# Performance work log

Hardware: AMD Instinct MI355X
Metric: run time of the kernel (lower is better)

Reference implementation:

```python
import jax, jax.numpy as jnp
import numpy as np

B, S, SE, D, H, F1, I, E, ND = 8, 512, 512, 1024, 16, 4096, 1024, 8, 4

def _ln(x, g, b, eps=1e-5):
    mu = x.mean(-1, keepdims=True)
    var = ((x - mu) ** 2).mean(-1, keepdims=True)
    return (x - mu) * jax.lax.rsqrt(var + eps) * g + b

def _mha(q_in, kv_in, qw, qb, kw, kb, vw, vb, ow, ob):
    b, sq, d = q_in.shape
    sk = kv_in.shape[1]
    dh = d // H
    scale = dh ** -0.5
    q = ((q_in @ qw.T + qb) * scale).reshape(b, sq, H, dh)
    k = (kv_in @ kw.T + kb).reshape(b, sk, H, dh)
    v = (kv_in @ vw.T + vb).reshape(b, sk, H, dh)
    attn = jax.nn.softmax(jnp.einsum('bqhd,bkhd->bhqk', q, k), axis=-1)
    o = jnp.einsum('bhqk,bkhd->bqhd', attn, v).reshape(b, sq, d)
    return o @ ow.T + ob

def setup_inputs():
    key = jax.random.key(0)
    ks = jax.random.split(key, 40)
    p = lambda i, sh: jax.random.normal(ks[i], sh, jnp.float32) * 0.02
    return {
        'hidden_states': jax.random.normal(ks[0], (B, S, D), jnp.float32),
        'encoder_hidden_states': jax.random.normal(ks[1], (B, SE, D), jnp.float32),
        'idxes': jax.random.randint(ks[2], (B,), 0, ND),
        'sa_qw': p(3, (D, D)), 'sa_qb': p(4, (D,)), 'sa_kw': p(5, (D, D)), 'sa_kb': p(6, (D,)),
        'sa_vw': p(7, (D, D)), 'sa_vb': p(8, (D,)), 'sa_ow': p(9, (D, D)), 'sa_ob': p(10, (D,)),
        'ca_qw': p(11, (D, D)), 'ca_qb': p(12, (D,)), 'ca_kw': p(13, (D, D)), 'ca_kb': p(14, (D,)),
        'ca_vw': p(15, (D, D)), 'ca_vb': p(16, (D,)), 'ca_ow': p(17, (D, D)), 'ca_ob': p(18, (D,)),
        'sa_ln_g': jnp.ones((D,), jnp.float32), 'sa_ln_b': jnp.zeros((D,), jnp.float32),
        'ca_ln_g': jnp.ones((D,), jnp.float32), 'ca_ln_b': jnp.zeros((D,), jnp.float32),
        'fin_ln_g': jnp.ones((D,), jnp.float32), 'fin_ln_b': jnp.zeros((D,), jnp.float32),
        'fc1_w': p(19, (F1, D)), 'fc1_b': p(20, (F1,)),
        'fc2_w': p(21, (D, F1)), 'fc2_b': p(22, (D,)),
        'exp1_w': p(23, (E, I, D)), 'exp1_b': p(24, (E, I)),
        'exp2_w': p(25, (E, D, I)),
        'gate_w': p(26, (ND, E, D)), 'gate_b': p(27, (ND, E)),
    }

def reference(hidden_states, encoder_hidden_states, idxes, sa_qw, sa_qb, sa_kw, sa_kb, sa_vw, sa_vb, sa_ow, sa_ob, ca_qw, ca_qb, ca_kw, ca_kb, ca_vw, ca_vb, ca_ow, ca_ob, sa_ln_g, sa_ln_b, ca_ln_g, ca_ln_b, fin_ln_g, fin_ln_b, fc1_w, fc1_b, fc2_w, fc2_b, exp1_w, exp1_b, exp2_w, gate_w, gate_b):
    # self-attention block
    res = hidden_states
    h = _mha(hidden_states, hidden_states, sa_qw, sa_qb, sa_kw, sa_kb, sa_vw, sa_vb, sa_ow, sa_ob)
    h = _ln(res + h, sa_ln_g, sa_ln_b)
    # cross-attention block
    res = h
    h = _mha(h, encoder_hidden_states, ca_qw, ca_qb, ca_kw, ca_kb, ca_vw, ca_vb, ca_ow, ca_ob)
    h = _ln(res + h, ca_ln_g, ca_ln_b)
    # dataset-gated MoE FFN (dropout=0 eval, margin_loss=False, keep_resident=True)
    bsz, seq, d = h.shape
    x = h.reshape(-1, d)                              # [T, D]
    tok_ds = jnp.repeat(idxes, seq)                   # [T] dataset id per token
    logits = jnp.einsum('ted,td->te', gate_w[tok_ds], x) + gate_b[tok_ds]
    probs = jax.nn.softmax(logits, axis=-1)
    gate = jnp.argmax(probs, axis=-1)                 # top-1 expert per token
    gate_value = jnp.max(probs, axis=-1)
    oh = jax.nn.one_hot(gate, E, dtype=x.dtype)       # [T, E] dispatch mask
    # effective expert fc1 = concat(fc1, expert_fc1): shared half + per-token expert half
    h1 = jax.nn.gelu(x @ fc1_w.T + fc1_b, approximate=False)                                  # [T, F1]
    h2 = jax.nn.gelu(jnp.einsum('td,te,eid->ti', x, oh, exp1_w) + exp1_b[gate], approximate=False)  # [T, I]
    # effective expert fc2 = concat(fc2, expert_fc2, dim=1), shared fc2 bias
    out = h1 @ fc2_w.T + jnp.einsum('ti,te,edi->td', h2, oh, exp2_w) + fc2_b                  # [T, D]
    out = out * gate_value[:, None]                   # keep_resident: scale before residual
    out = _ln(x + out, fin_ln_g, fin_ln_b)
    return out.reshape(bsz, seq, d)
```

## Files before the change

kernel.cpp:

```cpp
#include <hip/hip_runtime.h>
#include <math.h>

constexpr int cS = 512, cD = 1024, cH = 16, cDH = 64;
constexpr int cF1 = 4096, cI = 1024, cE = 8;
constexpr int cT = 4096;
constexpr long long TD = (long long)cT * cD;
constexpr long long WW = 1048576;

typedef __attribute__((ext_vector_type(8))) short bfrag;
typedef _Float16 f16x8 __attribute__((ext_vector_type(8)));
typedef __attribute__((ext_vector_type(4))) float f32x4;

__device__ __forceinline__ float gelu_exact(float x) {
  return 0.5f * x * (1.0f + erff(x * 0.70710678118654752440f));
}
__device__ __forceinline__ unsigned short f2b_rne(float x) {
  union { float f; unsigned u; } v; v.f = x;
  unsigned r = v.u + 0x7fffu + ((v.u >> 16) & 1u);
  return (unsigned short)(r >> 16);
}
__device__ __forceinline__ void split2(float v, unsigned short& h, unsigned short& m) {
  _Float16 hh = (_Float16)v;
  float r = v - (float)hh;
  _Float16 mm = (_Float16)r;
  union { _Float16 f; unsigned short u; } a, b;
  a.f = hh; b.f = mm;
  h = a.u; m = b.u;
}
__device__ __forceinline__ void async16(const void* g, void* l) {
  __builtin_amdgcn_global_load_lds(
      (const __attribute__((address_space(1))) unsigned int*)g,
      (__attribute__((address_space(3))) unsigned int*)l, 16, 0, 0);
}

template<int BM, int BN, int OUT_MODE, int AFP32>
__global__ __launch_bounds__(256) void mgemm2(
    const void* __restrict__ Ap, long long aPS, long long sA, int lda,
    const unsigned short* __restrict__ Bp, long long bPS, long long sB, int ldb,
    const float* __restrict__ bias,
    void* __restrict__ Cp, long long sC, int ldc,
    int K, float alpha, int zbase)
{
  constexpr int WM = BM / 2, WN = BN / 2, AI = WM / 16, BJ = WN / 16;
  constexpr int CA = AFP32 ? 0 : 2 * (BM / 16);
  constexpr int CB = 2 * (BN / 16);
  constexpr int CTOT = CA + CB;
  static_assert(CTOT % 4 == 0, "chunk count");
  constexpr int NCH = CTOT / 4;
  constexpr int FPT = (BM * 32) / 256;
  constexpr int TPR = 256 / BM;

  __shared__ unsigned short lA[2][BM * 32];
  __shared__ unsigned short lB[2][BN * 32];

  const int tid = threadIdx.x;
  const int w = tid >> 6, lane = tid & 63;
  const int z = blockIdx.z;
  const int m0 = blockIdx.x * BM, n0 = blockIdx.y * BN;
  const int wm = (w >> 1) * WM, wn = (w & 1) * WN;
  const int lr = lane >> 2, lc8 = (lane & 3) * 8;

  const unsigned short* gsrc[NCH];
  unsigned short* ldst[NCH];
#pragma unroll
  for (int ci = 0; ci < NCH; ++ci) {
    const int c = w + ci * 4;
    if (c < CA) {
      const int p = c / (BM / 16), cc = c % (BM / 16);
      const int row = cc * 16 + lr;
      gsrc[ci] = (const unsigned short*)Ap + p * aPS + (long long)z * sA
               + (long long)(m0 + row) * lda + lc8;
      ldst[ci] = &lA[p][cc * 16 * 32];
    } else {
      const int cb = c - CA;
      const int p = cb / (BN / 16), cc = cb % (BN / 16);
      const int row = cc * 16 + lr;
      gsrc[ci] = Bp + p * bPS + (long long)z * sB + (long long)(n0 + row) * ldb + lc8;
      ldst[ci] = &lB[p][cc * 16 * 32];
    }
  }
  const float* af32 = nullptr;
  int arow = 0, acol = 0;
  if constexpr (AFP32) {
    arow = tid / TPR; acol = (tid % TPR) * FPT;
    af32 = (const float*)Ap + (long long)z * sA + (long long)(m0 + arow) * lda + acol;
  }

  f32x4 acc[AI][BJ];
#pragma unroll
  for (int i = 0; i < AI; ++i)
#pragma unroll
    for (int j = 0; j < BJ; ++j) acc[i][j] = (f32x4){0.f, 0.f, 0.f, 0.f};

  for (int k0 = 0; k0 < K; k0 += 32) {
#pragma unroll
    for (int ci = 0; ci < NCH; ++ci) async16(gsrc[ci] + k0, ldst[ci]);
    if constexpr (AFP32) {
      float vv[FPT];
#pragma unroll
      for (int q4 = 0; q4 < FPT / 4; ++q4)
        *(float4*)&vv[q4 * 4] = *(const float4*)(af32 + k0 + q4 * 4);
      unsigned pk[2][FPT / 2];
#pragma unroll
      for (int q = 0; q < FPT / 2; ++q) {
        unsigned short h0, m0s, h1, m1s;
        split2(vv[2 * q], h0, m0s);
        split2(vv[2 * q + 1], h1, m1s);
        pk[0][q] = (unsigned)h0 | ((unsigned)h1 << 16);
        pk[1][q] = (unsigned)m0s | ((unsigned)m1s << 16);
      }
#pragma unroll
      for (int p = 0; p < 2; ++p) {
        unsigned* d = (unsigned*)&lA[p][arow * 32 + acol];
#pragma unroll
        for (int u = 0; u < FPT / 8; ++u)
          *(uint4*)(d + u * 4) = *(const uint4*)&pk[p][u * 4];
      }
    }
    asm volatile("s_waitcnt vmcnt(0)" ::: "memory");
    __syncthreads();

    f16x8 bf0[BJ], bf1[BJ], af[AI];
#pragma unroll
    for (int j = 0; j < BJ; ++j) {
      bf0[j] = *(const f16x8*)&lB[0][(wn + j * 16 + (lane & 15)) * 32 + (lane >> 4) * 8];
      bf1[j] = *(const f16x8*)&lB[1][(wn + j * 16 + (lane & 15)) * 32 + (lane >> 4) * 8];
    }
#pragma unroll
    for (int i = 0; i < AI; ++i)
      af[i] = *(const f16x8*)&lA[0][(wm + i * 16 + (lane & 15)) * 32 + (lane >> 4) * 8];
#pragma unroll
    for (int i = 0; i < AI; ++i)
#pragma unroll
      for (int j = 0; j < BJ; ++j)
        acc[i][j] = __builtin_amdgcn_mfma_f32_16x16x32_f16(af[i], bf0[j], acc[i][j], 0, 0, 0);
#pragma unroll
    for (int i = 0; i < AI; ++i)
#pragma unroll
      for (int j = 0; j < BJ; ++j)
        acc[i][j] = __builtin_amdgcn_mfma_f32_16x16x32_f16(af[i], bf1[j], acc[i][j], 0, 0, 0);
#pragma unroll
    for (int i = 0; i < AI; ++i)
      af[i] = *(const f16x8*)&lA[1][(wm + i * 16 + (lane & 15)) * 32 + (lane >> 4) * 8];
#pragma unroll
    for (int i = 0; i < AI; ++i)
#pragma unroll
      for (int j = 0; j < BJ; ++j)
        acc[i][j] = __builtin_amdgcn_mfma_f32_16x16x32_f16(af[i], bf0[j], acc[i][j], 0, 0, 0);
    __syncthreads();
  }

  const int zz = zbase + z;
#pragma unroll
  for (int i = 0; i < AI; ++i) {
#pragma unroll
    for (int r = 0; r < 4; ++r) {
      const int gm = m0 + wm + i * 16 + (lane >> 4) * 4 + r;
#pragma unroll
      for (int j = 0; j < BJ; ++j) {
        const int gn = n0 + wn + j * 16 + (lane & 15);
        float v = acc[i][j][r];
        if constexpr (OUT_MODE == 4) {
          v += bias[zz * cD + gn];
          unsigned short* C = (unsigned short*)Cp + (long long)zz * 2 * TD;
          const int b = gm >> 9, s = gm & 511, h = gn >> 6, dd = gn & 63;
          const long long idx = (((long long)(b * cH + h) * cS + s) << 6) + dd;
          unsigned short h_, m_;
          split2(v, h_, m_);
          C[idx] = h_; C[TD + idx] = m_;
        } else {
          if (bias) v += bias[gn];
          v *= alpha;
          long long idx;
          if constexpr (OUT_MODE == 0) {
            idx = (long long)z * sC + (long long)gm * ldc + gn;
          } else {
            const int b = zz >> 4, h = zz & 15;
            idx = ((long long)(b * cS + gm) << 10) + h * 64 + gn;
          }
          ((float*)Cp)[idx] = v;
        }
      }
    }
  }
}

__global__ __launch_bounds__(256) void transposeV(
    const unsigned short* __restrict__ src, unsigned short* __restrict__ dst)
{
  __shared__ unsigned short t[128 * 64];
  const int st = blockIdx.x;
  const int bh = blockIdx.y;
  const long long pl = (long long)blockIdx.z * TD;
  const unsigned short* Sp = src + pl + ((long long)bh * cS + st * 128) * cDH;
  const int tid = threadIdx.x;
  const int r0 = tid >> 3, c0 = (tid & 7) * 8;
#pragma unroll
  for (int i = 0; i < 4; ++i) {
    const int r = r0 + i * 32;
    uint4 v = *(const uint4*)(Sp + (long long)r * cDH + c0);
    *(uint4*)&t[r * 64 + (c0 ^ ((r & 7) << 3))] = v;
  }
  __syncthreads();
  const int dd = tid >> 2;
  unsigned short* Dp = dst + pl + (long long)(bh * cDH + dd) * cS + st * 128;
#pragma unroll
  for (int i = 0; i < 4; ++i) {
    const int s0 = ((tid & 3) + i * 4) * 8;
    alignas(16) unsigned short v[8];
#pragma unroll
    for (int j = 0; j < 8; ++j)
      v[j] = t[(s0 + j) * 64 + (dd ^ (j << 3))];
    *(uint4*)(Dp + s0) = *(const uint4*)v;
  }
}

template<int GATHER>
__global__ __launch_bounds__(256) void mgemm1(
    const unsigned short* __restrict__ A, int lda,
    const unsigned short* __restrict__ Bw, long long sB, int ldb,
    const float* __restrict__ bias, int sBias,
    void* __restrict__ Cp, int ldc,
    int K, int act, int obf, int accum,
    const int* __restrict__ token_list, const int* __restrict__ offsets)
{
  int m0, n0, beg = 0, cnt = 0x7fffffff;
  long long boff = 0;
  if constexpr (GATHER) {
    const int e = blockIdx.y;
    beg = offsets[e]; cnt = offsets[e + 1] - beg;
    m0 = blockIdx.z * 128;
    if (m0 >= cnt) return;
    n0 = blockIdx.x * 128;
    boff = (long long)e * sB;
    if (bias) bias += (long long)e * sBias;
  } else {
    m0 = blockIdx.x * 128; n0 = blockIdx.y * 128;
  }
  __shared__ unsigned short lA[128 * 32];
  __shared__ unsigned short lB[128 * 32];
  const int tid = threadIdx.x, w = tid >> 6, lane = tid & 63;
  const int wm = (w >> 1) * 64, wn = (w & 1) * 64;
  const int lr = lane >> 2, lc8 = (lane & 3) * 8;

  const unsigned short* gsrc[4];
  unsigned short* ldst[4];
#pragma unroll
  for (int ci = 0; ci < 4; ++ci) {
    const int c = w + ci * 4;
    if (c < 8) {
      const int row = c * 16 + lr;
      long long grow;
      if constexpr (GATHER) {
        int mr = m0 + row; if (mr >= cnt) mr = cnt - 1;
        grow = token_list[beg + mr];
      } else grow = m0 + row;
      gsrc[ci] = A + grow * (long long)lda + lc8;
      ldst[ci] = &lA[c * 16 * 32];
    } else {
      const int cc = c - 8;
      const int row = cc * 16 + lr;
      gsrc[ci] = Bw + boff + (long long)(n0 + row) * ldb + lc8;
      ldst[ci] = &lB[cc * 16 * 32];
    }
  }
  f32x4 acc[4][4];
#pragma unroll
  for (int i = 0; i < 4; ++i)
#pragma unroll
    for (int j = 0; j < 4; ++j) acc[i][j] = (f32x4){0.f, 0.f, 0.f, 0.f};

  for (int k0 = 0; k0 < K; k0 += 32) {
#pragma unroll
    for (int ci = 0; ci < 4; ++ci) async16(gsrc[ci] + k0, ldst[ci]);
    asm volatile("s_waitcnt vmcnt(0)" ::: "memory");
    __syncthreads();
    bfrag af[4], bf[4];
#pragma unroll
    for (int i = 0; i < 4; ++i)
      af[i] = *(const bfrag*)&lA[(wm + i * 16 + (lane & 15)) * 32 + (lane >> 4) * 8];
#pragma unroll
    for (int j = 0; j < 4; ++j)
      bf[j] = *(const bfrag*)&lB[(wn + j * 16 + (lane & 15)) * 32 + (lane >> 4) * 8];
#pragma unroll
    for (int i = 0; i < 4; ++i)
#pragma unroll
      for (int j = 0; j < 4; ++j)
        acc[i][j] = __builtin_amdgcn_mfma_f32_16x16x32_bf16(af[i], bf[j], acc[i][j], 0, 0, 0);
    __syncthreads();
  }

#pragma unroll
  for (int i = 0; i < 4; ++i) {
#pragma unroll
    for (int r = 0; r < 4; ++r) {
      const int ml = wm + i * 16 + (lane >> 4) * 4 + r;
      long long orow = 0; bool ok = true;
      if constexpr (GATHER) {
        if (m0 + ml < cnt) orow = token_list[beg + m0 + ml]; else ok = false;
      } else orow = m0 + ml;
      if (ok) {
#pragma unroll
        for (int j = 0; j < 4; ++j) {
          const int gn = n0 + wn + j * 16 + (lane & 15);
          float v = acc[i][j][r];
          if (bias) v += bias[gn];
          if (act) v = gelu_exact(v);
          const long long idx = orow * (long long)ldc + gn;
          if (obf) ((unsigned short*)Cp)[idx] = f2b_rne(v);
          else if (accum) ((float*)Cp)[idx] += v;
          else ((float*)Cp)[idx] = v;
        }
      }
    }
  }
}

__global__ __launch_bounds__(256) void softmax2(
    const float* __restrict__ Sc, unsigned short* __restrict__ P, long long pPS)
{
  const long long row = blockIdx.x;
  const int tid = threadIdx.x;
  const float* pr = Sc + row * cS;
  float2 v = *(const float2*)(pr + tid * 2);
  __shared__ float red[256];
  red[tid] = fmaxf(v.x, v.y);
  __syncthreads();
  for (int st = 128; st > 0; st >>= 1) { if (tid < st) red[tid] = fmaxf(red[tid], red[tid + st]); __syncthreads(); }
  const float M = red[0];
  __syncthreads();
  float e0 = expf(v.x - M), e1 = expf(v.y - M);
  red[tid] = e0 + e1;
  __syncthreads();
  for (int st = 128; st > 0; st >>= 1) { if (tid < st) red[tid] += red[tid + st]; __syncthreads(); }
  const float inv = 1.0f / red[0];
  e0 *= inv; e1 *= inv;
  unsigned short h0, m0s, h1, m1s;
  split2(e0, h0, m0s); split2(e1, h1, m1s);
  const long long o = row * cS + tid * 2;
  *(unsigned*)&P[o] = (unsigned)h0 | ((unsigned)h1 << 16);
  *(unsigned*)&P[pPS + o] = (unsigned)m0s | ((unsigned)m1s << 16);
}

__global__ __launch_bounds__(256) void addln_kernel(
    const float* __restrict__ ra, const float* __restrict__ rb,
    const float* __restrict__ rowscale,
    const float* __restrict__ g, const float* __restrict__ be,
    float* __restrict__ out, unsigned short* __restrict__ out16,
    int gate_on, const int* __restrict__ idxes,
    const float* __restrict__ gw, const float* __restrict__ gb,
    int* __restrict__ gate_idx, float* __restrict__ gate_val, int* __restrict__ counts)
{
  const int row = blockIdx.x, tid = threadIdx.x;
  const long long base = (long long)row * cD + tid * 4;
  const float sc = rowscale ? rowscale[row] : 1.0f;
  float4 va = *(const float4*)(ra + base);
  float4 vb = *(const float4*)(rb + base);
  float v[4] = { va.x + vb.x * sc, va.y + vb.y * sc, va.z + vb.z * sc, va.w + vb.w * sc };
  __shared__ float red[256];
  __shared__ float glog[8];
  red[tid] = v[0] + v[1] + v[2] + v[3];
  __syncthreads();
  for (int st = 128; st > 0; st >>= 1) { if (tid < st) red[tid] += red[tid + st]; __syncthreads(); }
  const float mu = red[0] * (1.0f / cD);
  __syncthreads();
  float vp = 0.f;
#pragma unroll
  for (int i = 0; i < 4; ++i) { float c = v[i] - mu; vp += c * c; }
  red[tid] = vp;
  __syncthreads();
  for (int st = 128; st > 0; st >>= 1) { if (tid < st) red[tid] += red[tid + st]; __syncthreads(); }
  const float rstd = 1.0f / sqrtf(red[0] * (1.0f / cD) + 1e-5f);
  __syncthreads();
  float4 gv = *(const float4*)(g + tid * 4);
  float4 bv = *(const float4*)(be + tid * 4);
  float x[4];
  x[0] = (v[0] - mu) * rstd * gv.x + bv.x;
  x[1] = (v[1] - mu) * rstd * gv.y + bv.y;
  x[2] = (v[2] - mu) * rstd * gv.z + bv.z;
  x[3] = (v[3] - mu) * rstd * gv.w + bv.w;
  if (out) {
    float4 o; o.x = x[0]; o.y = x[1]; o.z = x[2]; o.w = x[3];
    *(float4*)(out + base) = o;
  }
  if (out16) {
    uint2 uu;
    uu.x = (unsigned)f2b_rne(x[0]) | ((unsigned)f2b_rne(x[1]) << 16);
    uu.y = (unsigned)f2b_rne(x[2]) | ((unsigned)f2b_rne(x[3]) << 16);
    *(uint2*)(out16 + base) = uu;
  }
  if (gate_on) {
    const int ds = idxes[row >> 9];
    const float* gwr = gw + (long long)ds * (cE * cD);
    float part[8];
#pragma unroll
    for (int e = 0; e < 8; ++e) {
      float4 wv = *(const float4*)(gwr + e * cD + tid * 4);
      part[e] = x[0] * wv.x + x[1] * wv.y + x[2] * wv.z + x[3] * wv.w;
    }
    for (int e = 0; e < 8; ++e) {
      __syncthreads();
      red[tid] = part[e];
      __syncthreads();
      for (int st = 128; st > 0; st >>= 1) { if (tid < st) red[tid] += red[tid + st]; __syncthreads(); }
      if (tid == 0) glog[e] = red[0] + gb[ds * cE + e];
    }
    if (tid == 0) {
      float m = glog[0]; int arg = 0;
      for (int e = 1; e < 8; ++e) if (glog[e] > m) { m = glog[e]; arg = e; }
      float ssum = 0.f;
      for (int e = 0; e < 8; ++e) ssum += expf(glog[e] - m);
      gate_idx[row] = arg;
      gate_val[row] = 1.0f / ssum;
      atomicAdd(&counts[arg], 1);
    }
  }
}

__global__ __launch_bounds__(256) void conv2x4(
    const float* s0, const float* s1, const float* s2, const float* s3,
    unsigned short* dst, int n, float sc0)
{
  const int wsel = blockIdx.y;
  const float* s = (wsel == 0) ? s0 : (wsel == 1) ? s1 : (wsel == 2) ? s2 : s3;
  const float sc = (wsel == 0) ? sc0 : 1.0f;
  unsigned short* d = dst + (long long)wsel * 2 * n;
  const long long i = ((long long)blockIdx.x * 256 + threadIdx.x) * 4;
  if (i >= n) return;
  float4 v = *(const float4*)(s + i);
  float vv[4] = {v.x * sc, v.y * sc, v.z * sc, v.w * sc};
  unsigned short h[4], m[4];
#pragma unroll
  for (int q = 0; q < 4; ++q) split2(vv[q], h[q], m[q]);
  uint2 u;
  u.x = (unsigned)h[0] | ((unsigned)h[1] << 16); u.y = (unsigned)h[2] | ((unsigned)h[3] << 16);
  *(uint2*)&d[i] = u;
  u.x = (unsigned)m[0] | ((unsigned)m[1] << 16); u.y = (unsigned)m[2] | ((unsigned)m[3] << 16);
  *(uint2*)&d[n + i] = u;
}

__global__ __launch_bounds__(256) void conv1(const float* __restrict__ s,
                                             unsigned short* __restrict__ d, long long n)
{
  const long long i = ((long long)blockIdx.x * 256 + threadIdx.x) * 4;
  if (i >= n) return;
  float4 v = *(const float4*)(s + i);
  uint2 u;
  u.x = (unsigned)f2b_rne(v.x) | ((unsigned)f2b_rne(v.y) << 16);
  u.y = (unsigned)f2b_rne(v.z) | ((unsigned)f2b_rne(v.w) << 16);
  *(uint2*)&d[i] = u;
}

__global__ void prep_bias(const float* a0, const float* a1, const float* a2,
                          const float* b0, const float* b1, const float* b2,
                          float* dst)
{
  const int i = blockIdx.x * 256 + threadIdx.x;
  const int seg = i >> 10, off = i & 1023;
  const float* srcs[6] = {a0, a1, a2, b0, b1, b2};
  const float sc = (seg == 0 || seg == 3) ? 0.125f : 1.0f;
  dst[i] = srcs[seg][off] * sc;
}

__global__ void scan_kernel(const int* __restrict__ counts, int* __restrict__ offsets,
                            int* __restrict__ cursor)
{
  if (threadIdx.x == 0 && blockIdx.x == 0) {
    int a = 0;
    for (int e = 0; e < cE; ++e) { offsets[e] = a; cursor[e] = a; a += counts[e]; }
    offsets[cE] = a;
  }
}

__global__ __launch_bounds__(256) void scatter_kernel(
    const int* __restrict__ gate_idx, int* __restrict__ cursor, int* __restrict__ token_list)
{
  int t = blockIdx.x * 256 + threadIdx.x;
  if (t < cT) {
    int e = gate_idx[t];
    int slot = atomicAdd(&cursor[e], 1);
    token_list[slot] = t;
  }
}

extern "C" void kernel_launch(void* const* d_in, const int* in_sizes, int n_in,
                              void* d_out, int out_size, void* d_ws, size_t ws_size,
                              hipStream_t stream)
{
  (void)in_sizes; (void)n_in; (void)out_size;
  const float* hidden  = (const float*)d_in[0];
  const float* encoder = (const float*)d_in[1];
  const int*   idxes   = (const int*)d_in[2];
  const float* sa_qw = (const float*)d_in[3];
  const float* sa_qb = (const float*)d_in[4];
  const float* sa_kw = (const float*)d_in[5];
  const float* sa_kb = (const float*)d_in[6];
  const float* sa_vw = (const float*)d_in[7];
  const float* sa_vb = (const float*)d_in[8];
  const float* sa_ow = (const float*)d_in[9];
  const float* sa_ob = (const float*)d_in[10];
  const float* ca_qw = (const float*)d_in[11];
  const float* ca_qb = (const float*)d_in[12];
  const float* ca_kw = (const float*)d_in[13];
  const float* ca_kb = (const float*)d_in[14];
  const float* ca_vw = (const float*)d_in[15];
  const float* ca_vb = (const float*)d_in[16];
  const float* ca_ow = (const float*)d_in[17];
  const float* ca_ob = (const float*)d_in[18];
  const float* sa_ln_g = (const float*)d_in[19];
  const float* sa_ln_b = (const float*)d_in[20];
  const float* ca_ln_g = (const float*)d_in[21];
  const float* ca_ln_b = (const float*)d_in[22];
  const float* fin_ln_g = (const float*)d_in[23];
  const float* fin_ln_b = (const float*)d_in[24];
  const float* fc1_w = (const float*)d_in[25];
  const float* fc1_b = (const float*)d_in[26];
  const float* fc2_w = (const float*)d_in[27];
  const float* fc2_b = (const float*)d_in[28];
  const float* exp1_w = (const float*)d_in[29];
  const float* exp1_b = (const float*)d_in[30];
  const float* exp2_w = (const float*)d_in[31];
  const float* gate_w = (const float*)d_in[32];
  const float* gate_b = (const float*)d_in[33];
  float* out = (float*)d_out;

  size_t off = 0;
  auto alloc = [&](size_t bytes) {
    void* p = (char*)d_ws + off;
    off += (bytes + 255) & ~(size_t)255;
    return p;
  };
  unsigned short* wbuf = (unsigned short*)alloc(4ll * 2 * WW * 2);
  unsigned short* QKVs = (unsigned short*)alloc(4ll * 2 * TD * 2);
  float* attnO = (float*)alloc(TD * 4);
  float* hsa   = (float*)alloc(TD * 4);
  float* biasb = (float*)alloc(6 * cD * 4);
  float* gate_val = (float*)alloc(cT * 4);
  int* gate_idx   = (int*)alloc(cT * 4);
  int* token_list = (int*)alloc(cT * 4);
  int* ctl        = (int*)alloc(64 * 4);
  int* counts  = ctl;
  int* offsets = ctl + 16;
  int* cursor  = ctl + 32;
  const size_t off_x = off;
  float* xbuf = (float*)alloc(TD * 4);
  unsigned short* x16 = (unsigned short*)alloc(TD * 2);

  long long region_bytes = (long long)ws_size - (long long)off_x;
  long long perz = (long long)cS * cS * 8;
  int ZB = (int)(region_bytes / perz);
  if (ZB < 1) ZB = 1;
  if (ZB > 128) ZB = 128;
  float* scoresF = (float*)((char*)d_ws + off_x);
  unsigned short* Pp = (unsigned short*)((char*)d_ws + off_x + (long long)ZB * cS * cS * 4);
  const long long pPS = (long long)ZB * cS * cS;

  float* OdeltaF = (float*)QKVs;
  unsigned short* h1 = (unsigned short*)attnO;
  unsigned short* h2 = QKVs;
  float* moeF = (float*)(QKVs + 2 * WW * 4);

  dim3 blk(256);
  hipMemsetAsync(counts, 0, cE * sizeof(int), stream);
  prep_bias<<<dim3(24), blk, 0, stream>>>(sa_qb, sa_kb, sa_vb, ca_qb, ca_kb, ca_vb, biasb);

  auto attention = [&]() {
    for (int zb = 0; zb < 128; zb += ZB) {
      int zc = 128 - zb; if (zc > ZB) zc = ZB;
      mgemm2<128, 128, 0, 0><<<dim3(4, 4, zc), blk, 0, stream>>>(
          QKVs + (long long)zb * (cS * cDH), TD, (long long)cS * cDH, cDH,
          QKVs + 2 * TD + (long long)zb * (cS * cDH), TD, (long long)cS * cDH, cDH,
          nullptr, scoresF, (long long)cS * cS, cS, cDH, 1.0f, 0);
      softmax2<<<dim3(zc * cS), blk, 0, stream>>>(scoresF, Pp, pPS);
      mgemm2<128, 64, 2, 0><<<dim3(4, 1, zc), blk, 0, stream>>>(
          Pp, pPS, (long long)cS * cS, cS,
          QKVs + 6 * TD + (long long)zb * (cDH * cS), TD, (long long)cDH * cS, cS,
          nullptr, attnO, 0, 0, cS, 1.0f, zb);
    }
  };

  conv2x4<<<dim3(1024, 4), blk, 0, stream>>>(sa_qw, sa_kw, sa_vw, sa_ow, wbuf, (int)WW, 0.125f);
  mgemm2<64, 128, 4, 1><<<dim3(64, 8, 3), blk, 0, stream>>>(
      hidden, 0, 0, cD, wbuf, WW, 2 * WW, cD,
      biasb, QKVs, 0, 0, cD, 1.0f, 0);
  transposeV<<<dim3(4, 128, 2), blk, 0, stream>>>(QKVs + 4 * TD, QKVs + 6 * TD);
  attention();
  mgemm2<64, 128, 0, 1><<<dim3(64, 8, 1), blk, 0, stream>>>(
      attnO, 0, 0, cD, wbuf + 6ll * WW, WW, 0, cD,
      sa_ob, OdeltaF, 0, cD, cD, 1.0f, 0);
  addln_kernel<<<dim3(cT), blk, 0, stream>>>(
      hidden, OdeltaF, nullptr, sa_ln_g, sa_ln_b, hsa, nullptr,
      0, nullptr, nullptr, nullptr, nullptr, nullptr, nullptr);

  conv2x4<<<dim3(1024, 4), blk, 0, stream>>>(ca_qw, ca_kw, ca_vw, ca_ow, wbuf, (int)WW, 0.125f);
  mgemm2<64, 128, 4, 1><<<dim3(64, 8, 1), blk, 0, stream>>>(
      hsa, 0, 0, cD, wbuf, WW, 2 * WW, cD,
      biasb + 3 * cD, QKVs, 0, 0, cD, 1.0f, 0);
  mgemm2<64, 128, 4, 1><<<dim3(64, 8, 2), blk, 0, stream>>>(
      encoder, 0, 0, cD, wbuf + 2ll * WW, WW, 2 * WW, cD,
      biasb + 3 * cD, QKVs, 0, 0, cD, 1.0f, 1);
  transposeV<<<dim3(4, 128, 2), blk, 0, stream>>>(QKVs + 4 * TD, QKVs + 6 * TD);
  attention();
  mgemm2<64, 128, 0, 1><<<dim3(64, 8, 1), blk, 0, stream>>>(
      attnO, 0, 0, cD, wbuf + 6ll * WW, WW, 0, cD,
      ca_ob, OdeltaF, 0, cD, cD, 1.0f, 0);
  addln_kernel<<<dim3(cT), blk, 0, stream>>>(
      hsa, OdeltaF, nullptr, ca_ln_g, ca_ln_b, xbuf, x16,
      1, idxes, gate_w, gate_b, gate_idx, gate_val, counts);

  scan_kernel<<<dim3(1), dim3(64), 0, stream>>>(counts, offsets, cursor);
  scatter_kernel<<<dim3(16), blk, 0, stream>>>(gate_idx, cursor, token_list);

  unsigned short* wfc1 = wbuf;
  unsigned short* wfc2 = wbuf + 4194304;
  conv1<<<dim3(4096), blk, 0, stream>>>(fc1_w, wfc1, 4194304);
  conv1<<<dim3(4096), blk, 0, stream>>>(fc2_w, wfc2, 4194304);
  for (int tc = 0; tc < cT; tc += 2048) {
    mgemm1<0><<<dim3(16, 32), blk, 0, stream>>>(
        x16 + (long long)tc * cD, cD, wfc1, 0, cD, fc1_b, 0,
        h1, cF1, cD, 1, 1, 0, nullptr, nullptr);
    mgemm1<0><<<dim3(16, 8), blk, 0, stream>>>(
        h1, cF1, wfc2, 0, cF1, fc2_b, 0,
        moeF + (long long)tc * cD, cD, cF1, 0, 0, 0, nullptr, nullptr);
  }
  conv1<<<dim3(8192), blk, 0, stream>>>(exp1_w, wbuf, 8388608);
  mgemm1<1><<<dim3(8, 8, 32), blk, 0, stream>>>(
      x16, cD, wbuf, (long long)cI * cD, cD, exp1_b, cI,
      h2, cI, cD, 1, 1, 0, token_list, offsets);
  conv1<<<dim3(8192), blk, 0, stream>>>(exp2_w, wbuf, 8388608);
  mgemm1<1><<<dim3(8, 8, 32), blk, 0, stream>>>(
      h2, cI, wbuf, (long long)cD * cI, cI, nullptr, 0,
      moeF, cD, cI, 0, 0, 1, token_list, offsets);

  addln_kernel<<<dim3(cT), blk, 0, stream>>>(
      xbuf, moeF, gate_val, fin_ln_g, fin_ln_b, out, nullptr,
      0, nullptr, nullptr, nullptr, nullptr, nullptr, nullptr);
}
```

Baseline: 1.352 ms.

## Double-buffer GEMM LDS, pre-split fp32 activations, and use warp-per-row softmax/LayerNorm

```diff
diff --git a/kernel.cpp b/kernel.cpp
--- a/kernel.cpp
+++ b/kernel.cpp
@@ -32,26 +32,34 @@
       (const __attribute__((address_space(1))) unsigned int*)g,
       (__attribute__((address_space(3))) unsigned int*)l, 16, 0, 0);
 }
-
-template<int BM, int BN, int OUT_MODE, int AFP32>
+__device__ __forceinline__ float wsum(float v) {
+#pragma unroll
+  for (int off = 32; off; off >>= 1) v += __shfl_xor(v, off, 64);
+  return v;
+}
+__device__ __forceinline__ float wmax(float v) {
+#pragma unroll
+  for (int off = 32; off; off >>= 1) v = fmaxf(v, __shfl_xor(v, off, 64));
+  return v;
+}
+
+template<int BM, int BN, int OUT_MODE>
 __global__ __launch_bounds__(256) void mgemm2(
-    const void* __restrict__ Ap, long long aPS, long long sA, int lda,
+    const unsigned short* __restrict__ Ap, long long aPS, long long sA, int lda,
     const unsigned short* __restrict__ Bp, long long bPS, long long sB, int ldb,
     const float* __restrict__ bias,
     void* __restrict__ Cp, long long sC, int ldc,
     int K, float alpha, int zbase)
 {
   constexpr int WM = BM / 2, WN = BN / 2, AI = WM / 16, BJ = WN / 16;
-  constexpr int CA = AFP32 ? 0 : 2 * (BM / 16);
+  constexpr int CA = 2 * (BM / 16);
   constexpr int CB = 2 * (BN / 16);
   constexpr int CTOT = CA + CB;
   static_assert(CTOT % 4 == 0, "chunk count");
   constexpr int NCH = CTOT / 4;
-  constexpr int FPT = (BM * 32) / 256;
-  constexpr int TPR = 256 / BM;
-
-  __shared__ unsigned short lA[2][BM * 32];
-  __shared__ unsigned short lB[2][BN * 32];
+  constexpr int LT = (BM + BN) * 64;
+
+  __shared__ unsigned short lds[2][LT];
 
   const int tid = threadIdx.x;
   const int w = tid >> 6, lane = tid & 63;
@@ -61,29 +69,22 @@
   const int lr = lane >> 2, lc8 = (lane & 3) * 8;
 
   const unsigned short* gsrc[NCH];
-  unsigned short* ldst[NCH];
+  int loff[NCH];
 #pragma unroll
   for (int ci = 0; ci < NCH; ++ci) {
     const int c = w + ci * 4;
     if (c < CA) {
       const int p = c / (BM / 16), cc = c % (BM / 16);
       const int row = cc * 16 + lr;
-      gsrc[ci] = (const unsigned short*)Ap + p * aPS + (long long)z * sA
-               + (long long)(m0 + row) * lda + lc8;
-      ldst[ci] = &lA[p][cc * 16 * 32];
+      gsrc[ci] = Ap + p * aPS + (long long)z * sA + (long long)(m0 + row) * lda + lc8;
+      loff[ci] = p * (BM * 32) + cc * (16 * 32);
     } else {
       const int cb = c - CA;
       const int p = cb / (BN / 16), cc = cb % (BN / 16);
       const int row = cc * 16 + lr;
       gsrc[ci] = Bp + p * bPS + (long long)z * sB + (long long)(n0 + row) * ldb + lc8;
-      ldst[ci] = &lB[p][cc * 16 * 32];
-    }
-  }
-  const float* af32 = nullptr;
-  int arow = 0, acol = 0;
-  if constexpr (AFP32) {
-    arow = tid / TPR; acol = (tid % TPR) * FPT;
-    af32 = (const float*)Ap + (long long)z * sA + (long long)(m0 + arow) * lda + acol;
+      loff[ci] = 2 * (BM * 32) + p * (BN * 32) + cc * (16 * 32);
+    }
   }
 
   f32x4 acc[AI][BJ];
@@ -92,43 +93,30 @@
 #pragma unroll
     for (int j = 0; j < BJ; ++j) acc[i][j] = (f32x4){0.f, 0.f, 0.f, 0.f};
 
-  for (int k0 = 0; k0 < K; k0 += 32) {
-#pragma unroll
-    for (int ci = 0; ci < NCH; ++ci) async16(gsrc[ci] + k0, ldst[ci]);
-    if constexpr (AFP32) {
-      float vv[FPT];
-#pragma unroll
-      for (int q4 = 0; q4 < FPT / 4; ++q4)
-        *(float4*)&vv[q4 * 4] = *(const float4*)(af32 + k0 + q4 * 4);
-      unsigned pk[2][FPT / 2];
-#pragma unroll
-      for (int q = 0; q < FPT / 2; ++q) {
-        unsigned short h0, m0s, h1, m1s;
-        split2(vv[2 * q], h0, m0s);
-        split2(vv[2 * q + 1], h1, m1s);
-        pk[0][q] = (unsigned)h0 | ((unsigned)h1 << 16);
-        pk[1][q] = (unsigned)m0s | ((unsigned)m1s << 16);
-      }
-#pragma unroll
-      for (int p = 0; p < 2; ++p) {
-        unsigned* d = (unsigned*)&lA[p][arow * 32 + acol];
-#pragma unroll
-        for (int u = 0; u < FPT / 8; ++u)
-          *(uint4*)(d + u * 4) = *(const uint4*)&pk[p][u * 4];
-      }
-    }
-    asm volatile("s_waitcnt vmcnt(0)" ::: "memory");
-    __syncthreads();
+#pragma unroll
+  for (int ci = 0; ci < NCH; ++ci) async16(gsrc[ci], &lds[0][loff[ci]]);
+  __syncthreads();
+
+  int cur = 0;
+  for (int k0 = 32; k0 <= K; k0 += 32) {
+    if (k0 < K) {
+#pragma unroll
+      for (int ci = 0; ci < NCH; ++ci) async16(gsrc[ci] + k0, &lds[cur ^ 1][loff[ci]]);
+    }
+    const unsigned short* LA0 = &lds[cur][0];
+    const unsigned short* LA1 = &lds[cur][BM * 32];
+    const unsigned short* LB0 = &lds[cur][2 * (BM * 32)];
+    const unsigned short* LB1 = &lds[cur][2 * (BM * 32) + BN * 32];
 
     f16x8 bf0[BJ], bf1[BJ], af[AI];
 #pragma unroll
     for (int j = 0; j < BJ; ++j) {
-      bf0[j] = *(const f16x8*)&lB[0][(wn + j * 16 + (lane & 15)) * 32 + (lane >> 4) * 8];
-      bf1[j] = *(const f16x8*)&lB[1][(wn + j * 16 + (lane & 15)) * 32 + (lane >> 4) * 8];
+      bf0[j] = *(const f16x8*)&LB0[(wn + j * 16 + (lane & 15)) * 32 + (lane >> 4) * 8];
+      bf1[j] = *(const f16x8*)&LB1[(wn + j * 16 + (lane & 15)) * 32 + (lane >> 4) * 8];
     }
 #pragma unroll
     for (int i = 0; i < AI; ++i)
-      af[i] = *(const f16x8*)&lA[0][(wm + i * 16 + (lane & 15)) * 32 + (lane >> 4) * 8];
+      af[i] = *(const f16x8*)&LA0[(wm + i * 16 + (lane & 15)) * 32 + (lane >> 4) * 8];
 #pragma unroll
     for (int i = 0; i < AI; ++i)
 #pragma unroll
@@ -141,13 +129,14 @@
         acc[i][j] = __builtin_amdgcn_mfma_f32_16x16x32_f16(af[i], bf1[j], acc[i][j], 0, 0, 0);
 #pragma unroll
     for (int i = 0; i < AI; ++i)
-      af[i] = *(const f16x8*)&lA[1][(wm + i * 16 + (lane & 15)) * 32 + (lane >> 4) * 8];
+      af[i] = *(const f16x8*)&LA1[(wm + i * 16 + (lane & 15)) * 32 + (lane >> 4) * 8];
 #pragma unroll
     for (int i = 0; i < AI; ++i)
 #pragma unroll
       for (int j = 0; j < BJ; ++j)
         acc[i][j] = __builtin_amdgcn_mfma_f32_16x16x32_f16(af[i], bf0[j], acc[i][j], 0, 0, 0);
     __syncthreads();
+    cur ^= 1;
   }
 
   const int zz = zbase + z;
@@ -168,16 +157,17 @@
           unsigned short h_, m_;
           split2(v, h_, m_);
           C[idx] = h_; C[TD + idx] = m_;
+        } else if constexpr (OUT_MODE == 5) {
+          const int b = zz >> 4, h = zz & 15;
+          const long long idx = ((long long)(b * cS + gm) << 10) + h * 64 + gn;
+          unsigned short h_, m_;
+          split2(v, h_, m_);
+          ((unsigned short*)Cp)[idx] = h_;
+          ((unsigned short*)Cp)[sC + idx] = m_;
         } else {
           if (bias) v += bias[gn];
           v *= alpha;
-          long long idx;
-          if constexpr (OUT_MODE == 0) {
-            idx = (long long)z * sC + (long long)gm * ldc + gn;
-          } else {
-            const int b = zz >> 4, h = zz & 15;
-            idx = ((long long)(b * cS + gm) << 10) + h * 64 + gn;
-          }
+          const long long idx = (long long)z * sC + (long long)gm * ldc + gn;
           ((float*)Cp)[idx] = v;
         }
       }
@@ -237,14 +227,13 @@
   } else {
     m0 = blockIdx.x * 128; n0 = blockIdx.y * 128;
   }
-  __shared__ unsigned short lA[128 * 32];
-  __shared__ unsigned short lB[128 * 32];
+  __shared__ unsigned short lds[2][256 * 32];
   const int tid = threadIdx.x, w = tid >> 6, lane = tid & 63;
   const int wm = (w >> 1) * 64, wn = (w & 1) * 64;
   const int lr = lane >> 2, lc8 = (lane & 3) * 8;
 
   const unsigned short* gsrc[4];
-  unsigned short* ldst[4];
+  int loff[4];
 #pragma unroll
   for (int ci = 0; ci < 4; ++ci) {
     const int c = w + ci * 4;
@@ -256,12 +245,12 @@
         grow = token_list[beg + mr];
       } else grow = m0 + row;
       gsrc[ci] = A + grow * (long long)lda + lc8;
-      ldst[ci] = &lA[c * 16 * 32];
+      loff[ci] = c * (16 * 32);
     } else {
       const int cc = c - 8;
       const int row = cc * 16 + lr;
       gsrc[ci] = Bw + boff + (long long)(n0 + row) * ldb + lc8;
-      ldst[ci] = &lB[cc * 16 * 32];
+      loff[ci] = 128 * 32 + cc * (16 * 32);
     }
   }
   f32x4 acc[4][4];
@@ -270,11 +259,18 @@
 #pragma unroll
     for (int j = 0; j < 4; ++j) acc[i][j] = (f32x4){0.f, 0.f, 0.f, 0.f};
 
-  for (int k0 = 0; k0 < K; k0 += 32) {
-#pragma unroll
-    for (int ci = 0; ci < 4; ++ci) async16(gsrc[ci] + k0, ldst[ci]);
-    asm volatile("s_waitcnt vmcnt(0)" ::: "memory");
-    __syncthreads();
+#pragma unroll
+  for (int ci = 0; ci < 4; ++ci) async16(gsrc[ci], &lds[0][loff[ci]]);
+  __syncthreads();
+
+  int cur = 0;
+  for (int k0 = 32; k0 <= K; k0 += 32) {
+    if (k0 < K) {
+#pragma unroll
+      for (int ci = 0; ci < 4; ++ci) async16(gsrc[ci] + k0, &lds[cur ^ 1][loff[ci]]);
+    }
+    const unsigned short* lA = &lds[cur][0];
+    const unsigned short* lB = &lds[cur][128 * 32];
     bfrag af[4], bf[4];
 #pragma unroll
     for (int i = 0; i < 4; ++i)
@@ -288,6 +284,7 @@
       for (int j = 0; j < 4; ++j)
         acc[i][j] = __builtin_amdgcn_mfma_f32_16x16x32_bf16(af[i], bf[j], acc[i][j], 0, 0, 0);
     __syncthreads();
+    cur ^= 1;
   }
 
 #pragma unroll
@@ -319,27 +316,33 @@
 __global__ __launch_bounds__(256) void softmax2(
     const float* __restrict__ Sc, unsigned short* __restrict__ P, long long pPS)
 {
-  const long long row = blockIdx.x;
-  const int tid = threadIdx.x;
-  const float* pr = Sc + row * cS;
-  float2 v = *(const float2*)(pr + tid * 2);
-  __shared__ float red[256];
-  red[tid] = fmaxf(v.x, v.y);
-  __syncthreads();
-  for (int st = 128; st > 0; st >>= 1) { if (tid < st) red[tid] = fmaxf(red[tid], red[tid + st]); __syncthreads(); }
-  const float M = red[0];
-  __syncthreads();
-  float e0 = expf(v.x - M), e1 = expf(v.y - M);
-  red[tid] = e0 + e1;
-  __syncthreads();
-  for (int st = 128; st > 0; st >>= 1) { if (tid < st) red[tid] += red[tid + st]; __syncthreads(); }
-  const float inv = 1.0f / red[0];
-  e0 *= inv; e1 *= inv;
-  unsigned short h0, m0s, h1, m1s;
-  split2(e0, h0, m0s); split2(e1, h1, m1s);
-  const long long o = row * cS + tid * 2;
-  *(unsigned*)&P[o] = (unsigned)h0 | ((unsigned)h1 << 16);
-  *(unsigned*)&P[pPS + o] = (unsigned)m0s | ((unsigned)m1s << 16);
+  const int w = threadIdx.x >> 6, lane = threadIdx.x & 63;
+  const long long row = (long long)blockIdx.x * 4 + w;
+  const float* pr = Sc + row * cS + lane * 8;
+  float4 a = *(const float4*)pr;
+  float4 b = *(const float4*)(pr + 4);
+  float e[8] = {a.x, a.y, a.z, a.w, b.x, b.y, b.z, b.w};
+  float m = e[0];
+#pragma unroll
+  for (int q = 1; q < 8; ++q) m = fmaxf(m, e[q]);
+  m = wmax(m);
+  float s = 0.f;
+#pragma unroll
+  for (int q = 0; q < 8; ++q) { e[q] = expf(e[q] - m); s += e[q]; }
+  s = wsum(s);
+  const float inv = 1.0f / s;
+  unsigned h[4], mm[4];
+#pragma unroll
+  for (int q = 0; q < 4; ++q) {
+    unsigned short h0, m0s, h1, m1s;
+    split2(e[2 * q] * inv, h0, m0s);
+    split2(e[2 * q + 1] * inv, h1, m1s);
+    h[q] = (unsigned)h0 | ((unsigned)h1 << 16);
+    mm[q] = (unsigned)m0s | ((unsigned)m1s << 16);
+  }
+  const long long o = row * cS + lane * 8;
+  *(uint4*)&P[o] = *(const uint4*)h;
+  *(uint4*)&P[pPS + o] = *(const uint4*)mm;
 }
 
 __global__ __launch_bounds__(256) void addln_kernel(
@@ -347,69 +350,98 @@
     const float* __restrict__ rowscale,
     const float* __restrict__ g, const float* __restrict__ be,
     float* __restrict__ out, unsigned short* __restrict__ out16,
+    unsigned short* __restrict__ out2p,
     int gate_on, const int* __restrict__ idxes,
     const float* __restrict__ gw, const float* __restrict__ gb,
     int* __restrict__ gate_idx, float* __restrict__ gate_val, int* __restrict__ counts)
 {
-  const int row = blockIdx.x, tid = threadIdx.x;
-  const long long base = (long long)row * cD + tid * 4;
+  const int w = threadIdx.x >> 6, lane = threadIdx.x & 63;
+  const int row = blockIdx.x * 4 + w;
+  const long long base = (long long)row * cD + lane * 16;
   const float sc = rowscale ? rowscale[row] : 1.0f;
-  float4 va = *(const float4*)(ra + base);
-  float4 vb = *(const float4*)(rb + base);
-  float v[4] = { va.x + vb.x * sc, va.y + vb.y * sc, va.z + vb.z * sc, va.w + vb.w * sc };
-  __shared__ float red[256];
-  __shared__ float glog[8];
-  red[tid] = v[0] + v[1] + v[2] + v[3];
-  __syncthreads();
-  for (int st = 128; st > 0; st >>= 1) { if (tid < st) red[tid] += red[tid + st]; __syncthreads(); }
-  const float mu = red[0] * (1.0f / cD);
-  __syncthreads();
+  float v[16];
+#pragma unroll
+  for (int q = 0; q < 4; ++q) {
+    float4 a = *(const float4*)(ra + base + q * 4);
+    float4 b = *(const float4*)(rb + base + q * 4);
+    v[q * 4 + 0] = a.x + b.x * sc; v[q * 4 + 1] = a.y + b.y * sc;
+    v[q * 4 + 2] = a.z + b.z * sc; v[q * 4 + 3] = a.w + b.w * sc;
+  }
+  float s = 0.f;
+#pragma unroll
+  for (int q = 0; q < 16; ++q) s += v[q];
+  const float mu = wsum(s) * (1.0f / cD);
   float vp = 0.f;
 #pragma unroll
-  for (int i = 0; i < 4; ++i) { float c = v[i] - mu; vp += c * c; }
-  red[tid] = vp;
-  __syncthreads();
-  for (int st = 128; st > 0; st >>= 1) { if (tid < st) red[tid] += red[tid + st]; __syncthreads(); }
-  const float rstd = 1.0f / sqrtf(red[0] * (1.0f / cD) + 1e-5f);
-  __syncthreads();
-  float4 gv = *(const float4*)(g + tid * 4);
-  float4 bv = *(const float4*)(be + tid * 4);
-  float x[4];
-  x[0] = (v[0] - mu) * rstd * gv.x + bv.x;
-  x[1] = (v[1] - mu) * rstd * gv.y + bv.y;
-  x[2] = (v[2] - mu) * rstd * gv.z + bv.z;
-  x[3] = (v[3] - mu) * rstd * gv.w + bv.w;
+  for (int q = 0; q < 16; ++q) { float c = v[q] - mu; vp += c * c; }
+  const float rstd = 1.0f / sqrtf(wsum(vp) * (1.0f / cD) + 1e-5f);
+  float x[16];
+#pragma unroll
+  for (int q = 0; q < 4; ++q) {
+    float4 gv = *(const float4*)(g + lane * 16 + q * 4);
+    float4 bv = *(const float4*)(be + lane * 16 + q * 4);
+    x[q * 4 + 0] = (v[q * 4 + 0] - mu) * rstd * gv.x + bv.x;
+    x[q * 4 + 1] = (v[q * 4 + 1] - mu) * rstd * gv.y + bv.y;
+    x[q * 4 + 2] = (v[q * 4 + 2] - mu) * rstd * gv.z + bv.z;
+    x[q * 4 + 3] = (v[q * 4 + 3] - mu) * rstd * gv.w + bv.w;
+  }
   if (out) {
-    float4 o; o.x = x[0]; o.y = x[1]; o.z = x[2]; o.w = x[3];
-    *(float4*)(out + base) = o;
+#pragma unroll
+    for (int q = 0; q < 4; ++q) {
+      float4 o; o.x = x[q * 4]; o.y = x[q * 4 + 1]; o.z = x[q * 4 + 2]; o.w = x[q * 4 + 3];
+      *(float4*)(out + base + q * 4) = o;
+    }
   }
   if (out16) {
-    uint2 uu;
-    uu.x = (unsigned)f2b_rne(x[0]) | ((unsigned)f2b_rne(x[1]) << 16);
-    uu.y = (unsigned)f2b_rne(x[2]) | ((unsigned)f2b_rne(x[3]) << 16);
-    *(uint2*)(out16 + base) = uu;
+    unsigned u[8];
+#pragma unroll
+    for (int q = 0; q < 8; ++q)
+      u[q] = (unsigned)f2b_rne(x[2 * q]) | ((unsigned)f2b_rne(x[2 * q + 1]) << 16);
+    *(uint4*)&out16[base] = *(const uint4*)&u[0];
+    *(uint4*)&out16[base + 8] = *(const uint4*)&u[4];
+  }
+  if (out2p) {
+    unsigned uh[8], um[8];
+#pragma unroll
+    for (int q = 0; q < 8; ++q) {
+      unsigned short h0, m0s, h1, m1s;
+      split2(x[2 * q], h0, m0s);
+      split2(x[2 * q + 1], h1, m1s);
+      uh[q] = (unsigned)h0 | ((unsigned)h1 << 16);
+      um[q] = (unsigned)m0s | ((unsigned)m1s << 16);
+    }
+    *(uint4*)&out2p[base] = *(const uint4*)&uh[0];
+    *(uint4*)&out2p[base + 8] = *(const uint4*)&uh[4];
+    *(uint4*)&out2p[TD + base] = *(const uint4*)&um[0];
+    *(uint4*)&out2p[TD + base + 8] = *(const uint4*)&um[4];
   }
   if (gate_on) {
     const int ds = idxes[row >> 9];
-    const float* gwr = gw + (long long)ds * (cE * cD);
-    float part[8];
+    const float* gwr = gw + (long long)ds * (cE * cD) + lane * 16;
+    float glog[8];
 #pragma unroll
     for (int e = 0; e < 8; ++e) {
-      float4 wv = *(const float4*)(gwr + e * cD + tid * 4);
-      part[e] = x[0] * wv.x + x[1] * wv.y + x[2] * wv.z + x[3] * wv.w;
-    }
-    for (int e = 0; e < 8; ++e) {
-      __syncthreads();
-      red[tid] = part[e];
-      __syncthreads();
-      for (int st = 128; st > 0; st >>= 1) { if (tid < st) red[tid] += red[tid + st]; __syncthreads(); }
-      if (tid == 0) glog[e] = red[0] + gb[ds * cE + e];
-    }
-    if (tid == 0) {
-      float m = glog[0]; int arg = 0;
-      for (int e = 1; e < 8; ++e) if (glog[e] > m) { m = glog[e]; arg = e; }
+      float pe = 0.f;
+#pragma unroll
+      for (int q = 0; q < 4; ++q) {
+        float4 wv = *(const float4*)(gwr + e * cD + q * 4);
+        pe += x[q * 4] * wv.x + x[q * 4 + 1] * wv.y + x[q * 4 + 2] * wv.z + x[q * 4 + 3] * wv.w;
+      }
+      glog[e] = wsum(pe);
+    }
+    if (lane == 0) {
+      float m = glog[0] + gb[ds * cE];
+      int arg = 0;
+      float gl[8];
+      gl[0] = m;
+#pragma unroll
+      for (int e = 1; e < 8; ++e) {
+        gl[e] = glog[e] + gb[ds * cE + e];
+        if (gl[e] > m) { m = gl[e]; arg = e; }
+      }
       float ssum = 0.f;
-      for (int e = 0; e < 8; ++e) ssum += expf(glog[e] - m);
+#pragma unroll
+      for (int e = 0; e < 8; ++e) ssum += expf(gl[e] - m);
       gate_idx[row] = arg;
       gate_val[row] = 1.0f / ssum;
       atomicAdd(&counts[arg], 1);
@@ -432,6 +464,22 @@
   unsigned short h[4], m[4];
 #pragma unroll
   for (int q = 0; q < 4; ++q) split2(vv[q], h[q], m[q]);
+  uint2 u;
+  u.x = (unsigned)h[0] | ((unsigned)h[1] << 16); u.y = (unsigned)h[2] | ((unsigned)h[3] << 16);
+  *(uint2*)&d[i] = u;
+  u.x = (unsigned)m[0] | ((unsigned)m[1] << 16); u.y = (unsigned)m[2] | ((unsigned)m[3] << 16);
+  *(uint2*)&d[n + i] = u;
+}
+
+__global__ __launch_bounds__(256) void conv2p(const float* __restrict__ s,
+                                              unsigned short* __restrict__ d, long long n)
+{
+  const long long i = ((long long)blockIdx.x * 256 + threadIdx.x) * 4;
+  if (i >= n) return;
+  float4 v = *(const float4*)(s + i);
+  unsigned short h[4], m[4];
+  split2(v.x, h[0], m[0]); split2(v.y, h[1], m[1]);
+  split2(v.z, h[2], m[2]); split2(v.w, h[3], m[3]);
   uint2 u;
   u.x = (unsigned)h[0] | ((unsigned)h[1] << 16); u.y = (unsigned)h[2] | ((unsigned)h[3] << 16);
   *(uint2*)&d[i] = u;
@@ -532,7 +580,7 @@
   };
   unsigned short* wbuf = (unsigned short*)alloc(4ll * 2 * WW * 2);
   unsigned short* QKVs = (unsigned short*)alloc(4ll * 2 * TD * 2);
-  float* attnO = (float*)alloc(TD * 4);
+  unsigned short* attnO16 = (unsigned short*)alloc(2ll * TD * 2);
   float* hsa   = (float*)alloc(TD * 4);
   float* biasb = (float*)alloc(6 * cD * 4);
   float* gate_val = (float*)alloc(cT * 4);
@@ -555,8 +603,10 @@
   unsigned short* Pp = (unsigned short*)((char*)d_ws + off_x + (long long)ZB * cS * cS * 4);
   const long long pPS = (long long)ZB * cS * cS;
 
+  unsigned short* A16 = QKVs + 6 * TD;
+  unsigned short* hsa16 = attnO16;
   float* OdeltaF = (float*)QKVs;
-  unsigned short* h1 = (unsigned short*)attnO;
+  unsigned short* h1 = attnO16;
   unsigned short* h2 = QKVs;
   float* moeF = (float*)(QKVs + 2 * WW * 4);
 
@@ -567,45 +617,47 @@
   auto attention = [&]() {
     for (int zb = 0; zb < 128; zb += ZB) {
       int zc = 128 - zb; if (zc > ZB) zc = ZB;
-      mgemm2<128, 128, 0, 0><<<dim3(4, 4, zc), blk, 0, stream>>>(
+      mgemm2<128, 64, 0><<<dim3(4, 8, zc), blk, 0, stream>>>(
           QKVs + (long long)zb * (cS * cDH), TD, (long long)cS * cDH, cDH,
           QKVs + 2 * TD + (long long)zb * (cS * cDH), TD, (long long)cS * cDH, cDH,
           nullptr, scoresF, (long long)cS * cS, cS, cDH, 1.0f, 0);
-      softmax2<<<dim3(zc * cS), blk, 0, stream>>>(scoresF, Pp, pPS);
-      mgemm2<128, 64, 2, 0><<<dim3(4, 1, zc), blk, 0, stream>>>(
+      softmax2<<<dim3(zc * cS / 4), blk, 0, stream>>>(scoresF, Pp, pPS);
+      mgemm2<128, 64, 5><<<dim3(4, 1, zc), blk, 0, stream>>>(
           Pp, pPS, (long long)cS * cS, cS,
           QKVs + 6 * TD + (long long)zb * (cDH * cS), TD, (long long)cDH * cS, cS,
-          nullptr, attnO, 0, 0, cS, 1.0f, zb);
+          nullptr, attnO16, TD, 0, cS, 1.0f, zb);
     }
   };
 
   conv2x4<<<dim3(1024, 4), blk, 0, stream>>>(sa_qw, sa_kw, sa_vw, sa_ow, wbuf, (int)WW, 0.125f);
-  mgemm2<64, 128, 4, 1><<<dim3(64, 8, 3), blk, 0, stream>>>(
-      hidden, 0, 0, cD, wbuf, WW, 2 * WW, cD,
+  conv2p<<<dim3(4096), blk, 0, stream>>>(hidden, A16, TD);
+  mgemm2<64, 128, 4><<<dim3(64, 8, 3), blk, 0, stream>>>(
+      A16, TD, 0, cD, wbuf, WW, 2 * WW, cD,
       biasb, QKVs, 0, 0, cD, 1.0f, 0);
   transposeV<<<dim3(4, 128, 2), blk, 0, stream>>>(QKVs + 4 * TD, QKVs + 6 * TD);
   attention();
-  mgemm2<64, 128, 0, 1><<<dim3(64, 8, 1), blk, 0, stream>>>(
-      attnO, 0, 0, cD, wbuf + 6ll * WW, WW, 0, cD,
+  mgemm2<64, 128, 0><<<dim3(64, 8, 1), blk, 0, stream>>>(
+      attnO16, TD, 0, cD, wbuf + 6ll * WW, WW, 0, cD,
       sa_ob, OdeltaF, 0, cD, cD, 1.0f, 0);
-  addln_kernel<<<dim3(cT), blk, 0, stream>>>(
-      hidden, OdeltaF, nullptr, sa_ln_g, sa_ln_b, hsa, nullptr,
+  addln_kernel<<<dim3(cT / 4), blk, 0, stream>>>(
+      hidden, OdeltaF, nullptr, sa_ln_g, sa_ln_b, hsa, nullptr, hsa16,
       0, nullptr, nullptr, nullptr, nullptr, nullptr, nullptr);
 
   conv2x4<<<dim3(1024, 4), blk, 0, stream>>>(ca_qw, ca_kw, ca_vw, ca_ow, wbuf, (int)WW, 0.125f);
-  mgemm2<64, 128, 4, 1><<<dim3(64, 8, 1), blk, 0, stream>>>(
-      hsa, 0, 0, cD, wbuf, WW, 2 * WW, cD,
+  mgemm2<64, 128, 4><<<dim3(64, 8, 1), blk, 0, stream>>>(
+      hsa16, TD, 0, cD, wbuf, WW, 2 * WW, cD,
       biasb + 3 * cD, QKVs, 0, 0, cD, 1.0f, 0);
-  mgemm2<64, 128, 4, 1><<<dim3(64, 8, 2), blk, 0, stream>>>(
-      encoder, 0, 0, cD, wbuf + 2ll * WW, WW, 2 * WW, cD,
+  conv2p<<<dim3(4096), blk, 0, stream>>>(encoder, A16, TD);
+  mgemm2<64, 128, 4><<<dim3(64, 8, 2), blk, 0, stream>>>(
+      A16, TD, 0, cD, wbuf + 2ll * WW, WW, 2 * WW, cD,
       biasb + 3 * cD, QKVs, 0, 0, cD, 1.0f, 1);
   transposeV<<<dim3(4, 128, 2), blk, 0, stream>>>(QKVs + 4 * TD, QKVs + 6 * TD);
   attention();
-  mgemm2<64, 128, 0, 1><<<dim3(64, 8, 1), blk, 0, stream>>>(
-      attnO, 0, 0, cD, wbuf + 6ll * WW, WW, 0, cD,
+  mgemm2<64, 128, 0><<<dim3(64, 8, 1), blk, 0, stream>>>(
+      attnO16, TD, 0, cD, wbuf + 6ll * WW, WW, 0, cD,
       ca_ob, OdeltaF, 0, cD, cD, 1.0f, 0);
-  addln_kernel<<<dim3(cT), blk, 0, stream>>>(
-      hsa, OdeltaF, nullptr, ca_ln_g, ca_ln_b, xbuf, x16,
+  addln_kernel<<<dim3(cT / 4), blk, 0, stream>>>(
+      hsa, OdeltaF, nullptr, ca_ln_g, ca_ln_b, xbuf, x16, nullptr,
       1, idxes, gate_w, gate_b, gate_idx, gate_val, counts);
 
   scan_kernel<<<dim3(1), dim3(64), 0, stream>>>(counts, offsets, cursor);
@@ -632,7 +684,7 @@
       h2, cI, wbuf, (long long)cD * cI, cI, nullptr, 0,
       moeF, cD, cI, 0, 0, 1, token_list, offsets);
 
-  addln_kernel<<<dim3(cT), blk, 0, stream>>>(
-      xbuf, moeF, gate_val, fin_ln_g, fin_ln_b, out, nullptr,
+  addln_kernel<<<dim3(cT / 4), blk, 0, stream>>>(
+      xbuf, moeF, gate_val, fin_ln_g, fin_ln_b, out, nullptr, nullptr,
       0, nullptr, nullptr, nullptr, nullptr, nullptr, nullptr);
 }
```

Measured after the change: 1.207 ms. 1.12x faster.
